# Performance work log

Measured on AMD Instinct MI355X. Metric: run time of the kernel, lower is better.

The kernel has to match this reference:

```python
import jax, jax.numpy as jnp
import numpy as np

D_MODEL = 512
NHEAD = 8
D_K = D_MODEL // NHEAD
SCALE = float(np.sqrt(D_K))


def setup_inputs() -> dict:
    key = jax.random.key(0)
    ks = jax.random.split(key, 11)
    B, S = 2, 4096
    std = 1.0 / np.sqrt(D_MODEL)
    inp = {
        'q': jax.random.normal(ks[0], (B, S, D_MODEL), jnp.float32),
        'k': jax.random.normal(ks[1], (B, S, D_MODEL), jnp.float32),
        'v': jax.random.normal(ks[2], (B, S, D_MODEL), jnp.float32),
        'w_q': jax.random.normal(ks[3], (D_MODEL, D_MODEL), jnp.float32) * std,
        'b_q': jax.random.normal(ks[4], (D_MODEL,), jnp.float32) * std,
        'w_k': jax.random.normal(ks[5], (D_MODEL, D_MODEL), jnp.float32) * std,
        'b_k': jax.random.normal(ks[6], (D_MODEL,), jnp.float32) * std,
        'w_v': jax.random.normal(ks[7], (D_MODEL, D_MODEL), jnp.float32) * std,
        'b_v': jax.random.normal(ks[8], (D_MODEL,), jnp.float32) * std,
        'w_o': jax.random.normal(ks[9], (D_MODEL, D_MODEL), jnp.float32) * std,
        'b_o': jax.random.normal(ks[10], (D_MODEL,), jnp.float32) * std,
    }
    return inp


def reference(q, k, v, w_q, b_q, w_k, b_k, w_v, b_v, w_o, b_o):
    B, S, _ = q.shape
    # torch Linear: y = x @ W.T + b
    def proj(x, W, b):
        y = x @ W.T + b
        return y.reshape(B, -1, NHEAD, D_K).transpose(0, 2, 1, 3)  # [B,H,S,Dk]
    qh = proj(q, w_q, b_q)
    kh = proj(k, w_k, b_k)
    vh = proj(v, w_v, b_v)
    scores = jnp.einsum('bhsd,bhtd->bhst', qh, kh) / SCALE  # [B,H,S,S]
    attn = jax.nn.softmax(scores, axis=-1)
    out = jnp.einsum('bhst,bhtd->bhsd', attn, vh)  # [B,H,S,Dk]
    out = out.transpose(0, 2, 1, 3).reshape(B, S, D_MODEL)
    return out @ w_o.T + b_o
```

## Files before the change

### kernel.cpp

```cpp
#include <hip/hip_runtime.h>
#include <stdint.h>

#define DM 512
#define S_LEN 4096
#define NH 8
#define DK 64

typedef __attribute__((ext_vector_type(8))) short bf16x8;
typedef __attribute__((ext_vector_type(4))) float f32x4;

#define QSCALE 0.18033688011112042f
#define NEGBIAS -17.312340490667562f

__device__ inline ushort f2bf(float f) {
  union { float f; uint32_t u; } v; v.f = f;
  uint32_t r = v.u + 0x7fff + ((v.u >> 16) & 1);
  return (ushort)(r >> 16);
}
__device__ inline uint32_t fu(float f) {
  union { float f; uint32_t u; } v; v.f = f; return v.u;
}
__device__ inline uint32_t pktrunc(float lo, float hi) {
  return __builtin_amdgcn_perm(fu(hi), fu(lo), 0x07060302);
}

__device__ inline void async_cp16(const ushort* g, ushort* l) {
  __builtin_amdgcn_global_load_lds((const __attribute__((address_space(1))) void*)g,
                                   (__attribute__((address_space(3))) void*)l, 16, 0, 0);
}

__global__ __launch_bounds__(256) void cvt_w(const float4* __restrict__ s0, ushort* __restrict__ d0,
                                             const float4* __restrict__ s1, ushort* __restrict__ d1,
                                             const float4* __restrict__ s2, ushort* __restrict__ d2,
                                             const float4* __restrict__ s3, ushort* __restrict__ d3) {
  int i = blockIdx.x * 256 + threadIdx.x;
  {
    float4 v = s0[i];
    ushort4 o = {f2bf(v.x), f2bf(v.y), f2bf(v.z), f2bf(v.w)};
    *(ushort4*)&d0[i * 4] = o;
  }
  {
    float4 v = s1[i];
    ushort4 o = {f2bf(v.x), f2bf(v.y), f2bf(v.z), f2bf(v.w)};
    *(ushort4*)&d1[i * 4] = o;
  }
  {
    float4 v = s2[i];
    ushort4 o = {f2bf(v.x), f2bf(v.y), f2bf(v.z), f2bf(v.w)};
    *(ushort4*)&d2[i * 4] = o;
  }
  {
    float4 v = s3[i];
    ushort4 o = {f2bf(v.x), f2bf(v.y), f2bf(v.z), f2bf(v.w)};
    *(ushort4*)&d3[i * 4] = o;
  }
}

__global__ __launch_bounds__(256) void gemm_proj(
    const float* __restrict__ q, const float* __restrict__ k, const float* __restrict__ v,
    const ushort* __restrict__ wq, const ushort* __restrict__ wk, const ushort* __restrict__ wv,
    const float* __restrict__ bq, const float* __restrict__ bk, const float* __restrict__ bv,
    ushort* __restrict__ Qh, ushort* __restrict__ Kh, ushort* __restrict__ VhT) {
  const float* A; const ushort* Bt; const float* bias; float cs;
  if (blockIdx.z == 0)      { A = q; Bt = wq; bias = bq; cs = QSCALE; }
  else if (blockIdx.z == 1) { A = k; Bt = wk; bias = bk; cs = 1.0f; }
  else                      { A = v; Bt = wv; bias = bv; cs = 1.0f; }

  __shared__ ushort As[128 * 32];
  __shared__ ushort Bs[128 * 32];
  const int tid = threadIdx.x;
  const int w = tid >> 6, lane = tid & 63;
  const int quad = lane >> 4, l16 = lane & 15;
  const int wm = w >> 1, wn = w & 1;
  const int m0 = blockIdx.y * 128, n0 = blockIdx.x * 128;
  const f32x4 zero4 = {0.f, 0.f, 0.f, 0.f};

  f32x4 acc[4][4];
  #pragma unroll
  for (int i = 0; i < 4; i++)
    #pragma unroll
    for (int j = 0; j < 4; j++) acc[i][j] = zero4;

  for (int kb = 0; kb < 16; kb++) {
    const int k0 = kb * 32;
    #pragma unroll
    for (int r = 0; r < 2; r++) {
      int idx = r * 256 + tid;
      async_cp16(&Bt[(size_t)(n0 + (idx >> 2)) * DM + k0 + (idx & 3) * 8], &Bs[idx * 8]);
    }
    #pragma unroll
    for (int r = 0; r < 2; r++) {
      int idx = r * 256 + tid;
      int row = idx >> 2, col = (idx & 3) * 8;
      const float* src = &A[(size_t)(m0 + row) * DM + k0 + col];
      float4 a0 = *(const float4*)src;
      float4 a1 = *(const float4*)(src + 4);
      uint2 w0 = {pktrunc(a0.x, a0.y), pktrunc(a0.z, a0.w)};
      uint2 w1 = {pktrunc(a1.x, a1.y), pktrunc(a1.z, a1.w)};
      *(uint2*)&As[row * 32 + col] = w0;
      *(uint2*)&As[row * 32 + col + 4] = w1;
    }
    __syncthreads();
    bf16x8 af[4], bfr[4];
    #pragma unroll
    for (int i = 0; i < 4; i++) {
      af[i]  = *(const bf16x8*)&As[(wm * 64 + i * 16 + l16) * 32 + quad * 8];
      bfr[i] = *(const bf16x8*)&Bs[(wn * 64 + i * 16 + l16) * 32 + quad * 8];
    }
    #pragma unroll
    for (int i = 0; i < 4; i++)
      #pragma unroll
      for (int j = 0; j < 4; j++)
        acc[i][j] = __builtin_amdgcn_mfma_f32_16x16x32_bf16(af[i], bfr[j], acc[i][j], 0, 0, 0);
    __syncthreads();
  }

  if (blockIdx.z != 2) {
    ushort* C = (blockIdx.z == 0) ? Qh : Kh;
    #pragma unroll
    for (int j = 0; j < 4; j++) {
      int col_g = n0 + wn * 64 + j * 16 + l16;
      float bv = bias[col_g];
      int h = col_g >> 6, d = col_g & 63;
      #pragma unroll
      for (int i = 0; i < 4; i++) {
        #pragma unroll
        for (int r = 0; r < 4; r++) {
          int row_g = m0 + wm * 64 + i * 16 + quad * 4 + r;
          int b = row_g >> 12, s = row_g & 4095;
          C[(((size_t)(b * NH + h) << 12) + s) * DK + d] = f2bf((acc[i][j][r] + bv) * cs);
        }
      }
    }
  } else {
    #pragma unroll
    for (int j = 0; j < 4; j++) {
      int col_g = n0 + wn * 64 + j * 16 + l16;
      float bv = bias[col_g];
      int h = col_g >> 6, d = col_g & 63;
      #pragma unroll
      for (int i = 0; i < 4; i++) {
        int row0 = m0 + wm * 64 + i * 16 + quad * 4;
        int b = row0 >> 12, s0 = row0 & 4095;
        int sl = s0 & 31;
        int sp = (s0 & ~31) | (((sl >> 2) & 3) << 3) | (((sl >> 4) & 1) << 2);
        ushort4 pk = {f2bf(acc[i][j][0] + bv), f2bf(acc[i][j][1] + bv),
                      f2bf(acc[i][j][2] + bv), f2bf(acc[i][j][3] + bv)};
        *(ushort4*)&VhT[((size_t)(b * NH + h) * DK + d) * S_LEN + sp] = pk;
      }
    }
  }
}

__global__ __launch_bounds__(256) void gemm_out(const ushort* __restrict__ A,
                                                const ushort* __restrict__ Bt,
                                                const float* __restrict__ bias,
                                                float* __restrict__ C) {
  __shared__ ushort As[128 * 32];
  __shared__ ushort Bs[128 * 32];
  const int tid = threadIdx.x;
  const int w = tid >> 6, lane = tid & 63;
  const int quad = lane >> 4, l16 = lane & 15;
  const int wm = w >> 1, wn = w & 1;
  const int m0 = blockIdx.y * 128, n0 = blockIdx.x * 128;
  const f32x4 zero4 = {0.f, 0.f, 0.f, 0.f};

  f32x4 acc[4][4];
  #pragma unroll
  for (int i = 0; i < 4; i++)
    #pragma unroll
    for (int j = 0; j < 4; j++) acc[i][j] = zero4;

  for (int kb = 0; kb < 16; kb++) {
    const int k0 = kb * 32;
    #pragma unroll
    for (int r = 0; r < 2; r++) {
      int idx = r * 256 + tid;
      async_cp16(&A [(size_t)(m0 + (idx >> 2)) * DM + k0 + (idx & 3) * 8], &As[idx * 8]);
      async_cp16(&Bt[(size_t)(n0 + (idx >> 2)) * DM + k0 + (idx & 3) * 8], &Bs[idx * 8]);
    }
    __syncthreads();
    bf16x8 af[4], bfr[4];
    #pragma unroll
    for (int i = 0; i < 4; i++) {
      af[i]  = *(const bf16x8*)&As[(wm * 64 + i * 16 + l16) * 32 + quad * 8];
      bfr[i] = *(const bf16x8*)&Bs[(wn * 64 + i * 16 + l16) * 32 + quad * 8];
    }
    #pragma unroll
    for (int i = 0; i < 4; i++)
      #pragma unroll
      for (int j = 0; j < 4; j++)
        acc[i][j] = __builtin_amdgcn_mfma_f32_16x16x32_bf16(af[i], bfr[j], acc[i][j], 0, 0, 0);
    __syncthreads();
  }

  #pragma unroll
  for (int j = 0; j < 4; j++) {
    int col_g = n0 + wn * 64 + j * 16 + l16;
    float bv = bias[col_g];
    #pragma unroll
    for (int i = 0; i < 4; i++) {
      #pragma unroll
      for (int r = 0; r < 4; r++) {
        int row_g = m0 + wm * 64 + i * 16 + quad * 4 + r;
        C[(size_t)row_g * DM + col_g] = acc[i][j][r] + bv;
      }
    }
  }
}

__global__ __launch_bounds__(512, 4) void attn(const ushort* __restrict__ Qh,
                                               const ushort* __restrict__ Kh,
                                               const ushort* __restrict__ VhT,
                                               ushort* __restrict__ O) {
  __shared__ ushort smem[2][16384];
  const int tid = threadIdx.x;
  const int w = tid >> 6, lane = tid & 63;
  const int quad = lane >> 4, l16 = lane & 15;
  const int half = w >> 2;
  const int qw = w & 3;
  const int bh = blockIdx.x;
  const int q0 = blockIdx.y * 128 + qw * 32;
  const size_t base = (size_t)bh * S_LEN * DK;
  const f32x4 zero4 = {0.f, 0.f, 0.f, 0.f};
  const f32x4 negb = {NEGBIAS, NEGBIAS, NEGBIAS, NEGBIAS};
  const short one_bf = (short)0x3F80;
  const bf16x8 ones = {one_bf, one_bf, one_bf, one_bf, one_bf, one_bf, one_bf, one_bf};

  bf16x8 qf[2][2];
  #pragma unroll
  for (int i = 0; i < 2; i++)
    #pragma unroll
    for (int c = 0; c < 2; c++)
      qf[i][c] = *(const bf16x8*)&Qh[base + (size_t)(q0 + i * 16 + l16) * DK + c * 32 + quad * 8];

  f32x4 o[2][4];
  f32x4 l_acc[2];
  #pragma unroll
  for (int i = 0; i < 2; i++) {
    l_acc[i] = zero4;
    #pragma unroll
    for (int n = 0; n < 4; n++) o[i][n] = zero4;
  }

  #define STAGE(IT, BUF) do {                                                         \
    const int t0_ = (IT) * 128;                                                       \
    _Pragma("unroll")                                                                 \
    for (int r_ = 0; r_ < 2; r_++) {                                                  \
      int idx = r_ * 512 + tid;                                                       \
      int row = idx >> 3;                                                             \
      int cl = ((idx & 7) << 4) ^ ((row & 7) << 4);                                   \
      async_cp16(&Kh[base + (size_t)(t0_ + row) * DK + (cl >> 1)], &smem[BUF][idx * 8]); \
    }                                                                                 \
    _Pragma("unroll")                                                                 \
    for (int r_ = 0; r_ < 2; r_++) {                                                  \
      int idx = r_ * 512 + tid;                                                       \
      int row = idx >> 4;                                                             \
      int cl = ((idx & 15) << 4) ^ ((row & 7) << 4);                                  \
      async_cp16(&VhT[base + (size_t)row * S_LEN + t0_ + (cl >> 1)], &smem[BUF][8192 + idx * 8]); \
    }                                                                                 \
  } while (0)

  STAGE(0, 0);
  __syncthreads();

  const int swz = (l16 & 7) << 4;

  for (int it = 0; it < 32; it++) {
    const int cur = it & 1;
    if (it < 31) STAGE(it + 1, cur ^ 1);
    const ushort* Kb = &smem[cur][0];
    const ushort* Vb = &smem[cur][8192];

    bf16x8 kf[4][2];
    #pragma unroll
    for (int s = 0; s < 4; s++) {
      int row = half * 64 + s * 16 + l16;
      kf[s][0] = *(const bf16x8*)&Kb[row * 64 + ((( 0 + quad * 16) ^ swz) >> 1)];
      kf[s][1] = *(const bf16x8*)&Kb[row * 64 + (((64 + quad * 16) ^ swz) >> 1)];
    }
    f32x4 sc[2][4];
    __builtin_amdgcn_s_setprio(1);
    #pragma unroll
    for (int i = 0; i < 2; i++)
      #pragma unroll
      for (int s = 0; s < 4; s++) {
        f32x4 t = negb;
        t = __builtin_amdgcn_mfma_f32_16x16x32_bf16(kf[s][0], qf[i][0], t, 0, 0, 0);
        t = __builtin_amdgcn_mfma_f32_16x16x32_bf16(kf[s][1], qf[i][1], t, 0, 0, 0);
        sc[i][s] = t;
      }
    __builtin_amdgcn_s_setprio(0);
    float p[2][4][4];
    #pragma unroll
    for (int i = 0; i < 2; i++)
      #pragma unroll
      for (int s = 0; s < 4; s++)
        #pragma unroll
        for (int r = 0; r < 4; r++)
          p[i][s][r] = __builtin_amdgcn_exp2f(sc[i][s][r]);
    union { bf16x8 v; uint32_t u[4]; } pf[2][2];
    #pragma unroll
    for (int i = 0; i < 2; i++)
      #pragma unroll
      for (int ppl = 0; ppl < 2; ppl++) {
        int s0 = ppl * 2, s1 = ppl * 2 + 1;
        pf[i][ppl].u[0] = pktrunc(p[i][s0][0], p[i][s0][1]);
        pf[i][ppl].u[1] = pktrunc(p[i][s0][2], p[i][s0][3]);
        pf[i][ppl].u[2] = pktrunc(p[i][s1][0], p[i][s1][1]);
        pf[i][ppl].u[3] = pktrunc(p[i][s1][2], p[i][s1][3]);
        l_acc[i] = __builtin_amdgcn_mfma_f32_16x16x32_bf16(pf[i][ppl].v, ones, l_acc[i], 0, 0, 0);
      }
    bf16x8 vf[4][2];
    #pragma unroll
    for (int n = 0; n < 4; n++) {
      int row = n * 16 + l16;
      #pragma unroll
      for (int ppl = 0; ppl < 2; ppl++)
        vf[n][ppl] = *(const bf16x8*)&Vb[row * 128 + ((((half * 2 + ppl) * 64 + quad * 16) ^ swz) >> 1)];
    }
    __builtin_amdgcn_s_setprio(1);
    #pragma unroll
    for (int n = 0; n < 4; n++)
      #pragma unroll
      for (int ppl = 0; ppl < 2; ppl++)
        #pragma unroll
        for (int i = 0; i < 2; i++)
          o[i][n] = __builtin_amdgcn_mfma_f32_16x16x32_bf16(pf[i][ppl].v, vf[n][ppl], o[i][n], 0, 0, 0);
    __builtin_amdgcn_s_setprio(0);

    __syncthreads();
  }

  float* red = (float*)smem;
  const int roff = (qw * 64 + lane) * 40;
  if (half == 1) {
    #pragma unroll
    for (int i = 0; i < 2; i++) {
      #pragma unroll
      for (int n = 0; n < 4; n++)
        *(f32x4*)&red[roff + (i * 4 + n) * 4] = o[i][n];
      *(f32x4*)&red[roff + 32 + i * 4] = l_acc[i];
    }
  }
  __syncthreads();
  if (half == 0) {
    #pragma unroll
    for (int i = 0; i < 2; i++) {
      #pragma unroll
      for (int n = 0; n < 4; n++)
        o[i][n] += *(const f32x4*)&red[roff + (i * 4 + n) * 4];
      l_acc[i] += *(const f32x4*)&red[roff + 32 + i * 4];
    }
    const int b = bh >> 3, h = bh & 7;
    #pragma unroll
    for (int i = 0; i < 2; i++) {
      #pragma unroll
      for (int r = 0; r < 4; r++) {
        float inv = 1.0f / l_acc[i][r];
        int qq = q0 + i * 16 + quad * 4 + r;
        #pragma unroll
        for (int n = 0; n < 4; n++) {
          int d = n * 16 + l16;
          O[(size_t)(b * S_LEN + qq) * DM + h * DK + d] = f2bf(o[i][n][r] * inv);
        }
      }
    }
  }
}

extern "C" void kernel_launch(void* const* d_in, const int* in_sizes, int n_in,
                              void* d_out, int out_size, void* d_ws, size_t ws_size,
                              hipStream_t stream) {
  const float* q   = (const float*)d_in[0];
  const float* k   = (const float*)d_in[1];
  const float* v   = (const float*)d_in[2];
  const float* w_q = (const float*)d_in[3];
  const float* b_q = (const float*)d_in[4];
  const float* w_k = (const float*)d_in[5];
  const float* b_k = (const float*)d_in[6];
  const float* w_v = (const float*)d_in[7];
  const float* b_v = (const float*)d_in[8];
  const float* w_o = (const float*)d_in[9];
  const float* b_o = (const float*)d_in[10];

  const size_t W_ELEMS = (size_t)DM * DM;
  const size_t HEADS_ELEMS = (size_t)2 * NH * S_LEN * DK;
  ushort* wqb = (ushort*)d_ws;
  ushort* wkb = wqb + W_ELEMS;
  ushort* wvb = wkb + W_ELEMS;
  ushort* wob = wvb + W_ELEMS;
  ushort* Qh  = wob + W_ELEMS;
  ushort* Kh  = Qh + HEADS_ELEMS;
  ushort* VhT = Kh + HEADS_ELEMS;
  ushort* AttO = VhT + HEADS_ELEMS;

  cvt_w<<<256, 256, 0, stream>>>((const float4*)w_q, wqb, (const float4*)w_k, wkb,
                                 (const float4*)w_v, wvb, (const float4*)w_o, wob);
  gemm_proj<<<dim3(4, 64, 3), 256, 0, stream>>>(q, k, v, wqb, wkb, wvb,
                                                b_q, b_k, b_v, Qh, Kh, VhT);
  attn<<<dim3(16, 32), 512, 0, stream>>>(Qh, Kh, VhT, AttO);
  gemm_out<<<dim3(4, 64), 256, 0, stream>>>(AttO, wob, b_o, (float*)d_out);
}
```

Before: 225.6 us.

## Software-pipeline attention loop so PV of previous tile overlaps current exp

Restructures the flash-attention main loop so the P·V MFMAs of the previous key tile are interleaved with the exp2 computations of the current tile's scores. K tiles stay double-buffered while V tiles become triple-buffered, so the previous tile's V survives while the next tile is prefetched. Probabilities are ping-ponged between two register sets, with a prologue and an epilogue. The aim is to hide transcendental latency behind matrix work. The cost is extra LDS (80KB vs 64KB) and more live registers, which could hurt occupancy or cause spills.

Measured after the change: 311.4 us. 38.0% more time.

```diff
diff --git a/kernel.cpp b/kernel.cpp
--- a/kernel.cpp
+++ b/kernel.cpp
@@ -209,11 +209,13 @@
   }
 }
 
+typedef union { bf16x8 v; uint32_t u[4]; } pfu;
+
 __global__ __launch_bounds__(512, 4) void attn(const ushort* __restrict__ Qh,
                                                const ushort* __restrict__ Kh,
                                                const ushort* __restrict__ VhT,
                                                ushort* __restrict__ O) {
-  __shared__ ushort smem[2][16384];
+  __shared__ ushort smem[5][8192];
   const int tid = threadIdx.x;
   const int w = tid >> 6, lane = tid & 63;
   const int quad = lane >> 4, l16 = lane & 15;
@@ -243,94 +245,119 @@
     for (int n = 0; n < 4; n++) o[i][n] = zero4;
   }
 
-  #define STAGE(IT, BUF) do {                                                         \
+  #define STAGE(IT) do {                                                              \
     const int t0_ = (IT) * 128;                                                       \
+    ushort* kb_ = &smem[(IT) & 1][0];                                                 \
+    ushort* vb_ = &smem[2 + (IT) % 3][0];                                             \
     _Pragma("unroll")                                                                 \
     for (int r_ = 0; r_ < 2; r_++) {                                                  \
       int idx = r_ * 512 + tid;                                                       \
       int row = idx >> 3;                                                             \
       int cl = ((idx & 7) << 4) ^ ((row & 7) << 4);                                   \
-      async_cp16(&Kh[base + (size_t)(t0_ + row) * DK + (cl >> 1)], &smem[BUF][idx * 8]); \
+      async_cp16(&Kh[base + (size_t)(t0_ + row) * DK + (cl >> 1)], &kb_[idx * 8]);    \
     }                                                                                 \
     _Pragma("unroll")                                                                 \
     for (int r_ = 0; r_ < 2; r_++) {                                                  \
       int idx = r_ * 512 + tid;                                                       \
       int row = idx >> 4;                                                             \
       int cl = ((idx & 15) << 4) ^ ((row & 7) << 4);                                  \
-      async_cp16(&VhT[base + (size_t)row * S_LEN + t0_ + (cl >> 1)], &smem[BUF][8192 + idx * 8]); \
+      async_cp16(&VhT[base + (size_t)row * S_LEN + t0_ + (cl >> 1)], &vb_[8192 * 0 + idx * 8]); \
     }                                                                                 \
   } while (0)
 
-  STAGE(0, 0);
+  const int swz = (l16 & 7) << 4;
+
+  #define TILE_BODY(T, PFP, PFC, DO_PV) do {                                          \
+    if ((T) < 31) STAGE((T) + 1);                                                     \
+    const ushort* Kb = &smem[(T) & 1][0];                                             \
+    const ushort* Vp = &smem[2 + ((T) + 2) % 3][0];                       \
+    f32x4 sc[2][4];                                                                   \
+    __builtin_amdgcn_s_setprio(1);                                                    \
+    _Pragma("unroll")                                                                 \
+    for (int s_ = 0; s_ < 4; s_++) {                                                  \
+      int row_ = half * 64 + s_ * 16 + l16;                                           \
+      bf16x8 k0_ = *(const bf16x8*)&Kb[row_ * 64 + ((( 0 + quad * 16) ^ swz) >> 1)];  \
+      bf16x8 k1_ = *(const bf16x8*)&Kb[row_ * 64 + (((64 + quad * 16) ^ swz) >> 1)];  \
+      _Pragma("unroll")                                                               \
+      for (int i_ = 0; i_ < 2; i_++) {                                                \
+        f32x4 t_ = negb;                                                              \
+        t_ = __builtin_amdgcn_mfma_f32_16x16x32_bf16(k0_, qf[i_][0], t_, 0, 0, 0);    \
+        t_ = __builtin_amdgcn_mfma_f32_16x16x32_bf16(k1_, qf[i_][1], t_, 0, 0, 0);    \
+        sc[i_][s_] = t_;                                                              \
+      }                                                                               \
+    }                                                                                 \
+             \
+    _Pragma("unroll")                                                                 \
+    for (int ppl_ = 0; ppl_ < 2; ppl_++) {                                            \
+      bf16x8 vfh_[4];                                                                 \
+      if (DO_PV) {                                                                    \
+        _Pragma("unroll")                                                             \
+        for (int n_ = 0; n_ < 4; n_++)                                                \
+          vfh_[n_] = *(const bf16x8*)&Vp[(n_ * 16 + l16) * 128 +                      \
+                       ((((half * 2 + ppl_) * 64 + quad * 16) ^ swz) >> 1)];          \
+      }                                                                               \
+      _Pragma("unroll")                                                               \
+      for (int k_ = 0; k_ < 8; k_++) {                                                \
+        int s_ = (k_ >> 1) & 3, r_ = (k_ & 1) * 2;                                    \
+        sc[ppl_][s_][r_]     = __builtin_amdgcn_exp2f(sc[ppl_][s_][r_]);              \
+        sc[ppl_][s_][r_ + 1] = __builtin_amdgcn_exp2f(sc[ppl_][s_][r_ + 1]);          \
+        if (DO_PV) {                                                                  \
+          int n_ = k_ >> 1, ii_ = k_ & 1;                                             \
+          o[ii_][n_] = __builtin_amdgcn_mfma_f32_16x16x32_bf16(PFP[ii_][ppl_].v,      \
+                         vfh_[n_], o[ii_][n_], 0, 0, 0);                              \
+        }                                                                             \
+      }                                                                               \
+    }                                                                                 \
+    __builtin_amdgcn_s_setprio(0);                                                    \
+                                               \
+    _Pragma("unroll")                                                                 \
+    for (int i_ = 0; i_ < 2; i_++) {                                                  \
+      _Pragma("unroll")                                                               \
+      for (int ppl_ = 0; ppl_ < 2; ppl_++) {                                          \
+        int s0_ = ppl_ * 2, s1_ = ppl_ * 2 + 1;                                       \
+        PFC[i_][ppl_].u[0] = pktrunc(sc[i_][s0_][0], sc[i_][s0_][1]);                 \
+        PFC[i_][ppl_].u[1] = pktrunc(sc[i_][s0_][2], sc[i_][s0_][3]);                 \
+        PFC[i_][ppl_].u[2] = pktrunc(sc[i_][s1_][0], sc[i_][s1_][1]);                 \
+        PFC[i_][ppl_].u[3] = pktrunc(sc[i_][s1_][2], sc[i_][s1_][3]);                 \
+        l_acc[i_] = __builtin_amdgcn_mfma_f32_16x16x32_bf16(PFC[i_][ppl_].v, ones,    \
+                      l_acc[i_], 0, 0, 0);                                            \
+      }                                                                               \
+    }                                                                                 \
+    __syncthreads();                                                                  \
+  } while (0)
+
+  pfu pfA[2][2], pfB[2][2];
+
+  STAGE(0);
   __syncthreads();
 
-  const int swz = (l16 & 7) << 4;
-
-  for (int it = 0; it < 32; it++) {
-    const int cur = it & 1;
-    if (it < 31) STAGE(it + 1, cur ^ 1);
-    const ushort* Kb = &smem[cur][0];
-    const ushort* Vb = &smem[cur][8192];
-
-    bf16x8 kf[4][2];
-    #pragma unroll
-    for (int s = 0; s < 4; s++) {
-      int row = half * 64 + s * 16 + l16;
-      kf[s][0] = *(const bf16x8*)&Kb[row * 64 + ((( 0 + quad * 16) ^ swz) >> 1)];
-      kf[s][1] = *(const bf16x8*)&Kb[row * 64 + (((64 + quad * 16) ^ swz) >> 1)];
-    }
-    f32x4 sc[2][4];
+  TILE_BODY(0, pfB, pfA, 0);
+  for (int t = 1; t < 31; t += 2) {
+    TILE_BODY(t, pfA, pfB, 1);
+    TILE_BODY(t + 1, pfB, pfA, 1);
+  }
+  TILE_BODY(31, pfA, pfB, 1);
+
+  {
+    const ushort* Vp = &smem[3][0];
     __builtin_amdgcn_s_setprio(1);
     #pragma unroll
-    for (int i = 0; i < 2; i++)
-      #pragma unroll
-      for (int s = 0; s < 4; s++) {
-        f32x4 t = negb;
-        t = __builtin_amdgcn_mfma_f32_16x16x32_bf16(kf[s][0], qf[i][0], t, 0, 0, 0);
-        t = __builtin_amdgcn_mfma_f32_16x16x32_bf16(kf[s][1], qf[i][1], t, 0, 0, 0);
-        sc[i][s] = t;
-      }
+    for (int ppl = 0; ppl < 2; ppl++) {
+      bf16x8 vfh[4];
+      #pragma unroll
+      for (int n = 0; n < 4; n++)
+        vfh[n] = *(const bf16x8*)&Vp[(n * 16 + l16) * 128 +
+                   ((((half * 2 + ppl) * 64 + quad * 16) ^ swz) >> 1)];
+      #pragma unroll
+      for (int n = 0; n < 4; n++)
+        #pragma unroll
+        for (int ii = 0; ii < 2; ii++)
+          o[ii][n] = __builtin_amdgcn_mfma_f32_16x16x32_bf16(pfB[ii][ppl].v, vfh[n],
+                       o[ii][n], 0, 0, 0);
+    }
     __builtin_amdgcn_s_setprio(0);
-    float p[2][4][4];
-    #pragma unroll
-    for (int i = 0; i < 2; i++)
-      #pragma unroll
-      for (int s = 0; s < 4; s++)
-        #pragma unroll
-        for (int r = 0; r < 4; r++)
-          p[i][s][r] = __builtin_amdgcn_exp2f(sc[i][s][r]);
-    union { bf16x8 v; uint32_t u[4]; } pf[2][2];
-    #pragma unroll
-    for (int i = 0; i < 2; i++)
-      #pragma unroll
-      for (int ppl = 0; ppl < 2; ppl++) {
-        int s0 = ppl * 2, s1 = ppl * 2 + 1;
-        pf[i][ppl].u[0] = pktrunc(p[i][s0][0], p[i][s0][1]);
-        pf[i][ppl].u[1] = pktrunc(p[i][s0][2], p[i][s0][3]);
-        pf[i][ppl].u[2] = pktrunc(p[i][s1][0], p[i][s1][1]);
-        pf[i][ppl].u[3] = pktrunc(p[i][s1][2], p[i][s1][3]);
-        l_acc[i] = __builtin_amdgcn_mfma_f32_16x16x32_bf16(pf[i][ppl].v, ones, l_acc[i], 0, 0, 0);
-      }
-    bf16x8 vf[4][2];
-    #pragma unroll
-    for (int n = 0; n < 4; n++) {
-      int row = n * 16 + l16;
-      #pragma unroll
-      for (int ppl = 0; ppl < 2; ppl++)
-        vf[n][ppl] = *(const bf16x8*)&Vb[row * 128 + ((((half * 2 + ppl) * 64 + quad * 16) ^ swz) >> 1)];
-    }
-    __builtin_amdgcn_s_setprio(1);
-    #pragma unroll
-    for (int n = 0; n < 4; n++)
-      #pragma unroll
-      for (int ppl = 0; ppl < 2; ppl++)
-        #pragma unroll
-        for (int i = 0; i < 2; i++)
-          o[i][n] = __builtin_amdgcn_mfma_f32_16x16x32_bf16(pf[i][ppl].v, vf[n][ppl], o[i][n], 0, 0, 0);
-    __builtin_amdgcn_s_setprio(0);
-
-    __syncthreads();
-  }
+  }
+  __syncthreads();
 
   float* red = (float*)smem;
   const int roff = (qw * 64 + lane) * 40;
```

## Interleave exp2 with MFMA across query sub-tiles and remap blocks per XCD

Applied to the files above, without the earlier changes.

The attention inner loop is reordered so the exp2 work for one 16-row query sub-tile is issued between MFMAs of the other sub-tile, a software-pipelining step meant to overlap transcendental ALU work with matrix-core work. The setprio hints are removed. The grid is flattened to 1D and remapped so that consecutive blocks on the same XCD share (batch, head) pairs, which is meant to improve L2 reuse of K/V. This relies on the compiler keeping the interleaved order, and it raises register pressure.

After: 225.4 us. Within noise of the previous version (-0.1%).

```diff
diff --git a/kernel.cpp b/kernel.cpp
--- a/kernel.cpp
+++ b/kernel.cpp
@@ -209,6 +209,8 @@
   }
 }
 
+typedef union { bf16x8 v; uint32_t u[4]; } pfu;
+
 __global__ __launch_bounds__(512, 4) void attn(const ushort* __restrict__ Qh,
                                                const ushort* __restrict__ Kh,
                                                const ushort* __restrict__ VhT,
@@ -219,8 +221,10 @@
   const int quad = lane >> 4, l16 = lane & 15;
   const int half = w >> 2;
   const int qw = w & 3;
-  const int bh = blockIdx.x;
-  const int q0 = blockIdx.y * 128 + qw * 32;
+  const int lin = blockIdx.x;
+  const int xcd = lin & 7, slot = lin >> 3;
+  const int bh = (xcd << 1) | (slot & 1);
+  const int q0 = (slot >> 1) * 128 + qw * 32;
   const size_t base = (size_t)bh * S_LEN * DK;
   const f32x4 zero4 = {0.f, 0.f, 0.f, 0.f};
   const f32x4 negb = {NEGBIAS, NEGBIAS, NEGBIAS, NEGBIAS};
@@ -279,38 +283,36 @@
       kf[s][0] = *(const bf16x8*)&Kb[row * 64 + ((( 0 + quad * 16) ^ swz) >> 1)];
       kf[s][1] = *(const bf16x8*)&Kb[row * 64 + (((64 + quad * 16) ^ swz) >> 1)];
     }
-    f32x4 sc[2][4];
-    __builtin_amdgcn_s_setprio(1);
-    #pragma unroll
-    for (int i = 0; i < 2; i++)
-      #pragma unroll
-      for (int s = 0; s < 4; s++) {
-        f32x4 t = negb;
-        t = __builtin_amdgcn_mfma_f32_16x16x32_bf16(kf[s][0], qf[i][0], t, 0, 0, 0);
-        t = __builtin_amdgcn_mfma_f32_16x16x32_bf16(kf[s][1], qf[i][1], t, 0, 0, 0);
-        sc[i][s] = t;
-      }
-    __builtin_amdgcn_s_setprio(0);
-    float p[2][4][4];
-    #pragma unroll
-    for (int i = 0; i < 2; i++)
-      #pragma unroll
-      for (int s = 0; s < 4; s++)
-        #pragma unroll
-        for (int r = 0; r < 4; r++)
-          p[i][s][r] = __builtin_amdgcn_exp2f(sc[i][s][r]);
-    union { bf16x8 v; uint32_t u[4]; } pf[2][2];
-    #pragma unroll
-    for (int i = 0; i < 2; i++)
-      #pragma unroll
-      for (int ppl = 0; ppl < 2; ppl++) {
-        int s0 = ppl * 2, s1 = ppl * 2 + 1;
-        pf[i][ppl].u[0] = pktrunc(p[i][s0][0], p[i][s0][1]);
-        pf[i][ppl].u[1] = pktrunc(p[i][s0][2], p[i][s0][3]);
-        pf[i][ppl].u[2] = pktrunc(p[i][s1][0], p[i][s1][1]);
-        pf[i][ppl].u[3] = pktrunc(p[i][s1][2], p[i][s1][3]);
-        l_acc[i] = __builtin_amdgcn_mfma_f32_16x16x32_bf16(pf[i][ppl].v, ones, l_acc[i], 0, 0, 0);
-      }
+
+    f32x4 sc0[4], sc1[4];
+    #pragma unroll
+    for (int s = 0; s < 4; s++) {
+      f32x4 t = negb;
+      t = __builtin_amdgcn_mfma_f32_16x16x32_bf16(kf[s][0], qf[0][0], t, 0, 0, 0);
+      sc0[s] = __builtin_amdgcn_mfma_f32_16x16x32_bf16(kf[s][1], qf[0][1], t, 0, 0, 0);
+    }
+
+    #pragma unroll
+    for (int s = 0; s < 4; s++) {
+      f32x4 t = negb;
+      t = __builtin_amdgcn_mfma_f32_16x16x32_bf16(kf[s][0], qf[1][0], t, 0, 0, 0);
+      sc0[s][0] = __builtin_amdgcn_exp2f(sc0[s][0]);
+      sc0[s][1] = __builtin_amdgcn_exp2f(sc0[s][1]);
+      sc0[s][2] = __builtin_amdgcn_exp2f(sc0[s][2]);
+      sc0[s][3] = __builtin_amdgcn_exp2f(sc0[s][3]);
+      sc1[s] = __builtin_amdgcn_mfma_f32_16x16x32_bf16(kf[s][1], qf[1][1], t, 0, 0, 0);
+    }
+
+    pfu pf0[2];
+    #pragma unroll
+    for (int ppl = 0; ppl < 2; ppl++) {
+      int s0 = ppl * 2, s1 = ppl * 2 + 1;
+      pf0[ppl].u[0] = pktrunc(sc0[s0][0], sc0[s0][1]);
+      pf0[ppl].u[1] = pktrunc(sc0[s0][2], sc0[s0][3]);
+      pf0[ppl].u[2] = pktrunc(sc0[s1][0], sc0[s1][1]);
+      pf0[ppl].u[3] = pktrunc(sc0[s1][2], sc0[s1][3]);
+      l_acc[0] = __builtin_amdgcn_mfma_f32_16x16x32_bf16(pf0[ppl].v, ones, l_acc[0], 0, 0, 0);
+    }
     bf16x8 vf[4][2];
     #pragma unroll
     for (int n = 0; n < 4; n++) {
@@ -319,15 +321,31 @@
       for (int ppl = 0; ppl < 2; ppl++)
         vf[n][ppl] = *(const bf16x8*)&Vb[row * 128 + ((((half * 2 + ppl) * 64 + quad * 16) ^ swz) >> 1)];
     }
-    __builtin_amdgcn_s_setprio(1);
-    #pragma unroll
-    for (int n = 0; n < 4; n++)
-      #pragma unroll
-      for (int ppl = 0; ppl < 2; ppl++)
-        #pragma unroll
-        for (int i = 0; i < 2; i++)
-          o[i][n] = __builtin_amdgcn_mfma_f32_16x16x32_bf16(pf[i][ppl].v, vf[n][ppl], o[i][n], 0, 0, 0);
-    __builtin_amdgcn_s_setprio(0);
+
+    #pragma unroll
+    for (int ppl = 0; ppl < 2; ppl++) {
+      #pragma unroll
+      for (int n = 0; n < 4; n++) {
+        int e = ppl * 8 + n * 2;
+        sc1[e >> 2][e & 3]             = __builtin_amdgcn_exp2f(sc1[e >> 2][e & 3]);
+        sc1[(e + 1) >> 2][(e + 1) & 3] = __builtin_amdgcn_exp2f(sc1[(e + 1) >> 2][(e + 1) & 3]);
+        o[0][n] = __builtin_amdgcn_mfma_f32_16x16x32_bf16(pf0[ppl].v, vf[n][ppl], o[0][n], 0, 0, 0);
+      }
+    }
+
+    pfu pf1[2];
+    #pragma unroll
+    for (int ppl = 0; ppl < 2; ppl++) {
+      int s0 = ppl * 2, s1 = ppl * 2 + 1;
+      pf1[ppl].u[0] = pktrunc(sc1[s0][0], sc1[s0][1]);
+      pf1[ppl].u[1] = pktrunc(sc1[s0][2], sc1[s0][3]);
+      pf1[ppl].u[2] = pktrunc(sc1[s1][0], sc1[s1][1]);
+      pf1[ppl].u[3] = pktrunc(sc1[s1][2], sc1[s1][3]);
+      l_acc[1] = __builtin_amdgcn_mfma_f32_16x16x32_bf16(pf1[ppl].v, ones, l_acc[1], 0, 0, 0);
+      #pragma unroll
+      for (int n = 0; n < 4; n++)
+        o[1][n] = __builtin_amdgcn_mfma_f32_16x16x32_bf16(pf1[ppl].v, vf[n][ppl], o[1][n], 0, 0, 0);
+    }
 
     __syncthreads();
   }
@@ -399,6 +417,6 @@
                                  (const float4*)w_v, wvb, (const float4*)w_o, wob);
   gemm_proj<<<dim3(4, 64, 3), 256, 0, stream>>>(q, k, v, wqb, wkb, wvb,
                                                 b_q, b_k, b_v, Qh, Kh, VhT);
-  attn<<<dim3(16, 32), 512, 0, stream>>>(Qh, Kh, VhT, AttO);
+  attn<<<512, 512, 0, stream>>>(Qh, Kh, VhT, AttO);
   gemm_out<<<dim3(4, 64), 256, 0, stream>>>(AttO, wob, b_o, (float*)d_out);
 }
```

## Pre-convert q/k/v activations to bf16 and async-load them in projection GEMM

Applied to the files above, without the earlier changes.

The fp32-to-bf16 conversion of the q, k and v inputs moves out of the projection GEMM into an extended conversion kernel, and the GEMM now streams A tiles straight into LDS with async global_load_lds, the same way it loads the weights. The aim is to halve the activation bytes the GEMM reads and drop the register round-trip conversion from its inner loop. The cost is an extra full write and read of bf16 copies of the activations through workspace. Separately, attention blocks in the upper half of the grid now sleep briefly at start, apparently to stagger when blocks begin.

Result: faster. 216.4 us (-4.1%).

```diff
diff --git a/kernel.cpp b/kernel.cpp
--- a/kernel.cpp
+++ b/kernel.cpp
@@ -29,42 +29,41 @@
                                    (__attribute__((address_space(3))) void*)l, 16, 0, 0);
 }
 
-__global__ __launch_bounds__(256) void cvt_w(const float4* __restrict__ s0, ushort* __restrict__ d0,
-                                             const float4* __restrict__ s1, ushort* __restrict__ d1,
-                                             const float4* __restrict__ s2, ushort* __restrict__ d2,
-                                             const float4* __restrict__ s3, ushort* __restrict__ d3) {
-  int i = blockIdx.x * 256 + threadIdx.x;
-  {
-    float4 v = s0[i];
-    ushort4 o = {f2bf(v.x), f2bf(v.y), f2bf(v.z), f2bf(v.w)};
-    *(ushort4*)&d0[i * 4] = o;
-  }
-  {
-    float4 v = s1[i];
-    ushort4 o = {f2bf(v.x), f2bf(v.y), f2bf(v.z), f2bf(v.w)};
-    *(ushort4*)&d1[i * 4] = o;
-  }
-  {
-    float4 v = s2[i];
-    ushort4 o = {f2bf(v.x), f2bf(v.y), f2bf(v.z), f2bf(v.w)};
-    *(ushort4*)&d2[i * 4] = o;
-  }
-  {
-    float4 v = s3[i];
-    ushort4 o = {f2bf(v.x), f2bf(v.y), f2bf(v.z), f2bf(v.w)};
-    *(ushort4*)&d3[i * 4] = o;
+__global__ __launch_bounds__(256) void cvt_all(
+    const float4* __restrict__ s0, ushort* __restrict__ d0,
+    const float4* __restrict__ s1, ushort* __restrict__ d1,
+    const float4* __restrict__ s2, ushort* __restrict__ d2,
+    const float4* __restrict__ s3, ushort* __restrict__ d3,
+    const float4* __restrict__ x0, ushort* __restrict__ y0,
+    const float4* __restrict__ x1, ushort* __restrict__ y1,
+    const float4* __restrict__ x2, ushort* __restrict__ y2) {
+  if (blockIdx.x < 256) {
+    int i = blockIdx.x * 256 + threadIdx.x;
+    { float4 v = s0[i]; ushort4 o = {f2bf(v.x), f2bf(v.y), f2bf(v.z), f2bf(v.w)}; *(ushort4*)&d0[i * 4] = o; }
+    { float4 v = s1[i]; ushort4 o = {f2bf(v.x), f2bf(v.y), f2bf(v.z), f2bf(v.w)}; *(ushort4*)&d1[i * 4] = o; }
+    { float4 v = s2[i]; ushort4 o = {f2bf(v.x), f2bf(v.y), f2bf(v.z), f2bf(v.w)}; *(ushort4*)&d2[i * 4] = o; }
+    { float4 v = s3[i]; ushort4 o = {f2bf(v.x), f2bf(v.y), f2bf(v.z), f2bf(v.w)}; *(ushort4*)&d3[i * 4] = o; }
+  } else {
+    int b = blockIdx.x - 256;
+    #pragma unroll
+    for (int r = 0; r < 2; r++) {
+      int i = (b * 2 + r) * 256 + threadIdx.x;
+      { float4 v = x0[i]; ushort4 o = {f2bf(v.x), f2bf(v.y), f2bf(v.z), f2bf(v.w)}; *(ushort4*)&y0[i * 4] = o; }
+      { float4 v = x1[i]; ushort4 o = {f2bf(v.x), f2bf(v.y), f2bf(v.z), f2bf(v.w)}; *(ushort4*)&y1[i * 4] = o; }
+      { float4 v = x2[i]; ushort4 o = {f2bf(v.x), f2bf(v.y), f2bf(v.z), f2bf(v.w)}; *(ushort4*)&y2[i * 4] = o; }
+    }
   }
 }
 
 __global__ __launch_bounds__(256) void gemm_proj(
-    const float* __restrict__ q, const float* __restrict__ k, const float* __restrict__ v,
+    const ushort* __restrict__ xq, const ushort* __restrict__ xk, const ushort* __restrict__ xv,
     const ushort* __restrict__ wq, const ushort* __restrict__ wk, const ushort* __restrict__ wv,
     const float* __restrict__ bq, const float* __restrict__ bk, const float* __restrict__ bv,
     ushort* __restrict__ Qh, ushort* __restrict__ Kh, ushort* __restrict__ VhT) {
-  const float* A; const ushort* Bt; const float* bias; float cs;
-  if (blockIdx.z == 0)      { A = q; Bt = wq; bias = bq; cs = QSCALE; }
-  else if (blockIdx.z == 1) { A = k; Bt = wk; bias = bk; cs = 1.0f; }
-  else                      { A = v; Bt = wv; bias = bv; cs = 1.0f; }
+  const ushort* A; const ushort* Bt; const float* bias; float cs;
+  if (blockIdx.z == 0)      { A = xq; Bt = wq; bias = bq; cs = QSCALE; }
+  else if (blockIdx.z == 1) { A = xk; Bt = wk; bias = bk; cs = 1.0f; }
+  else                      { A = xv; Bt = wv; bias = bv; cs = 1.0f; }
 
   __shared__ ushort As[128 * 32];
   __shared__ ushort Bs[128 * 32];
@@ -86,19 +85,8 @@
     #pragma unroll
     for (int r = 0; r < 2; r++) {
       int idx = r * 256 + tid;
+      async_cp16(&A [(size_t)(m0 + (idx >> 2)) * DM + k0 + (idx & 3) * 8], &As[idx * 8]);
       async_cp16(&Bt[(size_t)(n0 + (idx >> 2)) * DM + k0 + (idx & 3) * 8], &Bs[idx * 8]);
-    }
-    #pragma unroll
-    for (int r = 0; r < 2; r++) {
-      int idx = r * 256 + tid;
-      int row = idx >> 2, col = (idx & 3) * 8;
-      const float* src = &A[(size_t)(m0 + row) * DM + k0 + col];
-      float4 a0 = *(const float4*)src;
-      float4 a1 = *(const float4*)(src + 4);
-      uint2 w0 = {pktrunc(a0.x, a0.y), pktrunc(a0.z, a0.w)};
-      uint2 w1 = {pktrunc(a1.x, a1.y), pktrunc(a1.z, a1.w)};
-      *(uint2*)&As[row * 32 + col] = w0;
-      *(uint2*)&As[row * 32 + col + 4] = w1;
     }
     __syncthreads();
     bf16x8 af[4], bfr[4];
@@ -208,6 +196,8 @@
     }
   }
 }
+
+typedef union { bf16x8 v; uint32_t u[4]; } pfu;
 
 __global__ __launch_bounds__(512, 4) void attn(const ushort* __restrict__ Qh,
                                                const ushort* __restrict__ Kh,
@@ -227,6 +217,11 @@
   const short one_bf = (short)0x3F80;
   const bf16x8 ones = {one_bf, one_bf, one_bf, one_bf, one_bf, one_bf, one_bf, one_bf};
 
+  if (blockIdx.y >= 16) {
+    #pragma unroll
+    for (int i = 0; i < 6; i++) __builtin_amdgcn_s_sleep(7);
+  }
+
   bf16x8 qf[2][2];
   #pragma unroll
   for (int i = 0; i < 2; i++)
@@ -299,7 +294,7 @@
         #pragma unroll
         for (int r = 0; r < 4; r++)
           p[i][s][r] = __builtin_amdgcn_exp2f(sc[i][s][r]);
-    union { bf16x8 v; uint32_t u[4]; } pf[2][2];
+    pfu pf[2][2];
     #pragma unroll
     for (int i = 0; i < 2; i++)
       #pragma unroll
@@ -385,19 +380,25 @@
   const float* b_o = (const float*)d_in[10];
 
   const size_t W_ELEMS = (size_t)DM * DM;
+  const size_t X_ELEMS = (size_t)2 * S_LEN * DM;
   const size_t HEADS_ELEMS = (size_t)2 * NH * S_LEN * DK;
   ushort* wqb = (ushort*)d_ws;
   ushort* wkb = wqb + W_ELEMS;
   ushort* wvb = wkb + W_ELEMS;
   ushort* wob = wvb + W_ELEMS;
-  ushort* Qh  = wob + W_ELEMS;
+  ushort* Xq  = wob + W_ELEMS;
+  ushort* Xk  = Xq + X_ELEMS;
+  ushort* Xv  = Xk + X_ELEMS;
+  ushort* Qh  = Xv + X_ELEMS;
   ushort* Kh  = Qh + HEADS_ELEMS;
   ushort* VhT = Kh + HEADS_ELEMS;
   ushort* AttO = VhT + HEADS_ELEMS;
 
-  cvt_w<<<256, 256, 0, stream>>>((const float4*)w_q, wqb, (const float4*)w_k, wkb,
-                                 (const float4*)w_v, wvb, (const float4*)w_o, wob);
-  gemm_proj<<<dim3(4, 64, 3), 256, 0, stream>>>(q, k, v, wqb, wkb, wvb,
+  cvt_all<<<2304, 256, 0, stream>>>((const float4*)w_q, wqb, (const float4*)w_k, wkb,
+                                    (const float4*)w_v, wvb, (const float4*)w_o, wob,
+                                    (const float4*)q, Xq, (const float4*)k, Xk,
+                                    (const float4*)v, Xv);
+  gemm_proj<<<dim3(4, 64, 3), 256, 0, stream>>>(Xq, Xk, Xv, wqb, wkb, wvb,
                                                 b_q, b_k, b_v, Qh, Kh, VhT);
   attn<<<dim3(16, 32), 512, 0, stream>>>(Qh, Kh, VhT, AttO);
   gemm_out<<<dim3(4, 64), 256, 0, stream>>>(AttO, wob, b_o, (float*)d_out);
```
